# Optimization experiments

Measured on AMD Instinct MI355X. Metric: run time of the kernel, lower is better.

The kernel has to match this reference:

```python
import jax, jax.numpy as jnp
import numpy as np

PATCH_ORIG = (5, 15, 15)
DWS = [(1, 4, 4), (1, 2, 2), (1, 1, 1)]
STRIDE = [(1, 6, 6), (1, 6, 6), (1, 3, 3)]
EMBED = 32
EPS = 1e-6


def _extract_full_patches(x, shape, stride):
    # x: (N,C,D,H,W) -> (N*P, C, *shape) patches (torch unfold + permute + view)
    N, C = x.shape[:2]
    sp = x.shape[2:]
    nb = tuple((sp[i] - shape[i]) // stride[i] + 1 for i in range(3))
    d = (jnp.arange(nb[0]) * stride[0])[:, None] + jnp.arange(shape[0])[None, :]
    h = (jnp.arange(nb[1]) * stride[1])[:, None] + jnp.arange(shape[1])[None, :]
    w = (jnp.arange(nb[2]) * stride[2])[:, None] + jnp.arange(shape[2])[None, :]
    pat = x[:, :, d[:, None, None, :, None, None],
                  h[None, :, None, None, :, None],
                  w[None, None, :, None, None, :]]
    # (N, C, nb0, nb1, nb2, p0, p1, p2) -> (N*P, C, p0, p1, p2)
    pat = pat.transpose(0, 2, 3, 4, 1, 5, 6, 7).reshape(-1, C, *shape)
    return pat, nb


def _extract_centers(x, stride, offset, nb):
    # 1x1x1 patches at fixed crop offset, limited to nb -> (N*P, C)
    sl = x[:, :, offset[0]::stride[0], offset[1]::stride[1], offset[2]::stride[2]]
    sl = sl[:, :, :nb[0], :nb[1], :nb[2]]
    N, C = sl.shape[:2]
    return sl.transpose(0, 2, 3, 4, 1).reshape(-1, C)


def _maxpool(x, fct):
    # MaxPool3d(kernel=stride=fct) on exactly-divisible dims via reshape trick
    B, C = x.shape[:2]
    p0, p1, p2 = x.shape[2] // fct[0], x.shape[3] // fct[1], x.shape[4] // fct[2]
    x = x.reshape(B, C, p0, fct[0], p1, fct[1], p2, fct[2])
    return x.max(axis=(3, 5, 7))


def _dice(pred, trg):
    # inferno SorensenDiceLoss, channelwise: flatten to (C, -1)
    p = pred.transpose(1, 0, 2, 3, 4).reshape(pred.shape[1], -1)
    t = trg.transpose(1, 0, 2, 3, 4).reshape(trg.shape[1], -1)
    num = (p * t).sum(-1)
    den = jnp.clip((p * p + t * t).sum(-1), EPS, None)
    return (-2.0 * num / den).sum()


def _level_loss(pred, target, W, b, lvl):
    gt = target[:, :1].astype(jnp.float32)           # GT label volume (N,1,D,H,W)
    affs = target[:, 1:].astype(jnp.float32)
    bnd = 1.0 - affs
    bmask = bnd[:, 4:].max(1, keepdims=True) if lvl == 0 else bnd[:, :4].max(1, keepdims=True)
    dws, stride = DWS[lvl], STRIDE[lvl]
    pshape = tuple(p * f for p, f in zip(PATCH_ORIG, dws))
    off = tuple(s // 2 for s in pshape)              # crop offset (rnd crop fixed to 0)

    gt_patches, nb = _extract_full_patches(gt, pshape, stride)   # (P,1,*pshape)
    centers = _extract_centers(gt, stride, off, nb)[:, 0]        # (P,)
    on_bnd = _extract_centers(bmask, stride, off, nb)[:, 0]      # (P,)

    me = (gt_patches != centers[:, None, None, None, None]).astype(jnp.float32)
    ign = (gt_patches == 0).astype(jnp.float32)
    valid = ((centers != 0) & (on_bnd != 1.0)).astype(jnp.float32)

    trg = _maxpool(me, dws)                                      # (P,1,*PATCH_ORIG)
    ign_m = _maxpool(ign, dws) > 0

    emb = _extract_centers(pred, stride, off, nb)                # (P, EMBED)
    pp = jax.nn.sigmoid(emb @ W + b).reshape(-1, 1, *PATCH_ORIG) # patch decoder

    pp = jnp.where(ign_m, 0.0, pp)
    trg = jnp.where(ign_m, 0.0, trg)
    v = valid[:, None, None, None, None]                         # mask == select valid patches for sum-based Dice
    return _dice(pp * v, trg * v)


def setup_inputs() -> dict:
    key = jax.random.key(0)
    ks = jax.random.split(key, 16)
    shapes = [(2, 8, 160, 160), (2, 8, 80, 80), (2, 8, 40, 40)]
    inp = {}
    for lvl, (n, d, hh, ww) in enumerate(shapes):
        inp[f'pred{lvl}'] = jax.random.normal(ks[lvl], (n, EMBED, d, hh, ww), jnp.float32)
        gt = jax.random.randint(ks[3 + lvl], (n, 1, d, hh, ww), 0, 50, jnp.int32)
        affs = jax.random.randint(ks[6 + lvl], (n, 8, d, hh, ww), 0, 2, jnp.int32)
        inp[f'tgt{lvl}'] = jnp.concatenate([gt, affs], axis=1)
        inp[f'W{lvl}'] = 0.1 * jax.random.normal(ks[9 + lvl], (EMBED, int(np.prod(PATCH_ORIG))), jnp.float32)
        inp[f'b{lvl}'] = jnp.zeros((int(np.prod(PATCH_ORIG)),), jnp.float32)
    return inp


def reference(pred0, pred1, pred2, W0, b0, W1, b1, W2, b2, tgt0, tgt1, tgt2):
    loss = _level_loss(pred0, tgt0, W0, b0, 0)
    loss = loss + _level_loss(pred1, tgt1, W1, b1, 1)
    loss = loss + _level_loss(pred2, tgt2, W2, b2, 2)
    return loss
```

## Files before the change

kernel.cpp:

```cpp
#include <hip/hip_runtime.h>
#include <hip/hip_bf16.h>


constexpr int NBATCH = 2;
constexpr int EMB = 32;
constexpr int TGTC = 9;
constexpr int PZ = 5, PY = 15, PX = 15;
constexpr int P = PZ * PY * PX;

constexpr int NBLK0 = NBATCH * 4 * 17 * 17;
constexpr int NBLK1 = NBATCH * 4 * 9 * 9;
constexpr int NBLK2 = NBATCH * 4 * 9 * 9;
constexpr int NBLK_TOT = NBLK0 + NBLK1 + NBLK2;

template <int D, int H, int W,
          int NB0, int NBH, int NBW,
          int SH, int SW,
          int DH, int DWIN,
          int OFFZ, int OFFY, int OFFX,
          int AFFB>
__device__ __forceinline__
void level_body(const int lbid,
                const float* __restrict__ pred,
                const int* __restrict__ tgt,
                const float* __restrict__ Wm,
                const float* __restrict__ bv,
                float* __restrict__ partials)
{
    const int tid = threadIdx.x;

    int k  = lbid % NBW;
    int t1 = lbid / NBW;
    int j  = t1 % NBH;
    int t2 = t1 / NBH;
    int i  = t2 % NB0;
    int b  = t2 / NB0;

    const int HW = H * W;
    const int CH = D * HW;
    const int zc = OFFZ + i;
    const int yc = OFFY + j * SH;
    const int xc = OFFX + k * SW;
    const int cidx = zc * HW + yc * W + xc;

    const int c = tgt[b * TGTC * CH + cidx];
    bool allaff = true;
    #pragma unroll
    for (int ch = 0; ch < 4; ++ch)
        allaff &= (tgt[(b * TGTC + AFFB + ch) * CH + cidx] != 0);
    const bool valid = (c != 0) && allaff;

    if (!valid) {
        if (tid == 0) {
            partials[2 * lbid]     = 0.0f;
            partials[2 * lbid + 1] = 0.0f;
        }
        return;
    }

    float ev[EMB];
    #pragma unroll
    for (int e = 0; e < EMB; ++e)
        ev[e] = pred[(b * EMB + e) * CH + cidx];

    const int* __restrict__ gtb = tgt + b * TGTC * CH;

    float num = 0.0f, den = 0.0f;
    for (int o = tid; o < P; o += 256) {
        const int pz = o / (PY * PX);
        const int r  = o - pz * (PY * PX);
        const int py = r / PX;
        const int px = r - py * PX;

        float dot = bv[o];
        #pragma unroll
        for (int e = 0; e < EMB; ++e)
            dot = fmaf(ev[e], Wm[e * P + o], dot);
        float pp = __builtin_amdgcn_rcpf(1.0f + __expf(-dot));

        const int zb = i + pz;
        const int yb = j * SH + py * DH;
        const int xb = k * SW + px * DWIN;
        bool anyz = false, anyd = false;
        #pragma unroll
        for (int wy = 0; wy < DH; ++wy) {
            #pragma unroll
            for (int wx = 0; wx < DWIN; ++wx) {
                const int g = gtb[zb * HW + (yb + wy) * W + (xb + wx)];
                anyz |= (g == 0);
                anyd |= (g != c);
            }
        }
        float trg = (anyz || !anyd) ? 0.0f : 1.0f;
        if (anyz) pp = 0.0f;

        num = fmaf(pp, trg, num);
        den += pp * pp + trg * trg;
    }

    #pragma unroll
    for (int off = 32; off > 0; off >>= 1) {
        num += __shfl_xor(num, off);
        den += __shfl_xor(den, off);
    }
    __shared__ float sn[4], sd[4];
    if ((tid & 63) == 0) { sn[tid >> 6] = num; sd[tid >> 6] = den; }
    __syncthreads();
    if (tid == 0) {
        partials[2 * lbid]     = sn[0] + sn[1] + sn[2] + sn[3];
        partials[2 * lbid + 1] = sd[0] + sd[1] + sd[2] + sd[3];
    }
}

__global__ __launch_bounds__(256)
void stage_kernel(const float* __restrict__ pred0, const int* __restrict__ tgt0,
                  const float* __restrict__ W0, const float* __restrict__ b0,
                  const float* __restrict__ pred1, const int* __restrict__ tgt1,
                  const float* __restrict__ W1, const float* __restrict__ b1,
                  const float* __restrict__ pred2, const int* __restrict__ tgt2,
                  const float* __restrict__ W2, const float* __restrict__ b2,
                  float* __restrict__ partials)
{
    const int gb = blockIdx.x;
    if (gb < NBLK0) {
        level_body<8, 160, 160, 4, 17, 17, 6, 6, 4, 4, 2, 30, 30, 5>(
            gb, pred0, tgt0, W0, b0, partials);
    } else if (gb < NBLK0 + NBLK1) {
        level_body<8, 80, 80, 4, 9, 9, 6, 6, 2, 2, 2, 15, 15, 1>(
            gb - NBLK0, pred1, tgt1, W1, b1, partials + 2 * NBLK0);
    } else {
        level_body<8, 40, 40, 4, 9, 9, 3, 3, 1, 1, 2, 7, 7, 1>(
            gb - NBLK0 - NBLK1, pred2, tgt2, W2, b2,
            partials + 2 * (NBLK0 + NBLK1));
    }
}

__global__ __launch_bounds__(512)
void finalize_kernel(const float* __restrict__ partials, float* __restrict__ out)
{
    const int tid = threadIdx.x;

    constexpr int NF4 = NBLK_TOT / 2;
    constexpr int B01 = NBLK0 / 2;
    constexpr int B12 = (NBLK0 + NBLK1) / 2;

    float n0 = 0.f, d0 = 0.f, n1 = 0.f, d1 = 0.f, n2 = 0.f, d2 = 0.f;
    const float4* p4 = (const float4*)partials;
    for (int p = tid; p < NF4; p += 512) {
        const float4 v = p4[p];
        if (p < B01)      { n0 += v.x + v.z; d0 += v.y + v.w; }
        else if (p < B12) { n1 += v.x + v.z; d1 += v.y + v.w; }
        else              { n2 += v.x + v.z; d2 += v.y + v.w; }
    }

    #pragma unroll
    for (int off = 32; off > 0; off >>= 1) {
        n0 += __shfl_down(n0, off);  d0 += __shfl_down(d0, off);
        n1 += __shfl_down(n1, off);  d1 += __shfl_down(d1, off);
        n2 += __shfl_down(n2, off);  d2 += __shfl_down(d2, off);
    }
    __shared__ float s[8][6];
    if ((tid & 63) == 0) {
        const int w = tid >> 6;
        s[w][0] = n0; s[w][1] = d0; s[w][2] = n1;
        s[w][3] = d1; s[w][4] = n2; s[w][5] = d2;
    }
    __syncthreads();
    if (tid == 0) {
        float acc[6];
        #pragma unroll
        for (int q = 0; q < 6; ++q) {
            acc[q] = s[0][q];
            #pragma unroll
            for (int w = 1; w < 8; ++w) acc[q] += s[w][q];
        }
        float loss = 0.0f;
        loss += -2.0f * acc[0] / fmaxf(acc[1], 1e-6f);
        loss += -2.0f * acc[2] / fmaxf(acc[3], 1e-6f);
        loss += -2.0f * acc[4] / fmaxf(acc[5], 1e-6f);
        out[0] = loss;
    }
}

extern "C" void kernel_launch(void* const* d_in, const int* in_sizes, int n_in,
                              void* d_out, int out_size, void* d_ws, size_t ws_size,
                              hipStream_t stream)
{
    const float* pred0 = (const float*)d_in[0];
    const int*   tgt0  = (const int*)  d_in[1];
    const float* W0    = (const float*)d_in[2];
    const float* b0    = (const float*)d_in[3];
    const float* pred1 = (const float*)d_in[4];
    const int*   tgt1  = (const int*)  d_in[5];
    const float* W1    = (const float*)d_in[6];
    const float* b1    = (const float*)d_in[7];
    const float* pred2 = (const float*)d_in[8];
    const int*   tgt2  = (const int*)  d_in[9];
    const float* W2    = (const float*)d_in[10];
    const float* b2    = (const float*)d_in[11];

    float* out      = (float*)d_out;
    float* partials = (float*)d_ws;

    stage_kernel<<<NBLK_TOT, 256, 0, stream>>>(
        pred0, tgt0, W0, b0, pred1, tgt1, W1, b1, pred2, tgt2, W2, b2,
        partials);
    finalize_kernel<<<1, 512, 0, stream>>>(partials, out);
}
```

Baseline: 18.89 us.

## Merge stage and finalize into one cooperative kernel with persistent blocks

Replaces the two-kernel launch with a single cooperative kernel of 256 persistent blocks. Each block strides over several patches, checks all their validity flags up front, and runs the heavy projection only for valid ones. Per-block per-level sums are then reduced after a grid-wide sync in block 0. This removes the second launch and the work of many short-lived invalid blocks, but serialises up to SMAX patches per block, which can cause load imbalance, and adds the cost of a grid barrier.

```diff
diff --git a/kernel.cpp b/kernel.cpp
--- a/kernel.cpp
+++ b/kernel.cpp
@@ -1,5 +1,8 @@
 #include <hip/hip_runtime.h>
 #include <hip/hip_bf16.h>
+#include <hip/hip_cooperative_groups.h>
+
+namespace cg = cooperative_groups;
 
 
 constexpr int NBATCH = 2;
@@ -13,57 +16,27 @@
 constexpr int NBLK2 = NBATCH * 4 * 9 * 9;
 constexpr int NBLK_TOT = NBLK0 + NBLK1 + NBLK2;
 
-template <int D, int H, int W,
-          int NB0, int NBH, int NBW,
-          int SH, int SW,
-          int DH, int DWIN,
-          int OFFZ, int OFFY, int OFFX,
-          int AFFB>
+constexpr int GRID = 256;
+constexpr int SMAX = (NBLK_TOT + GRID - 1) / GRID;
+
+template <int Wd, int HWd, int CHd,
+          int SH, int SW, int DH, int DW,
+          int OFFY, int OFFX>
 __device__ __forceinline__
-void level_body(const int lbid,
-                const float* __restrict__ pred,
-                const int* __restrict__ tgt,
-                const float* __restrict__ Wm,
-                const float* __restrict__ bv,
-                float* __restrict__ partials)
+void heavy(const int b, const int i, const int j, const int k, const int c,
+           const float* __restrict__ pred, const int* __restrict__ tgt,
+           const float* __restrict__ Wm, const float* __restrict__ bv,
+           float& num_o, float& den_o)
 {
     const int tid = threadIdx.x;
-
-    int k  = lbid % NBW;
-    int t1 = lbid / NBW;
-    int j  = t1 % NBH;
-    int t2 = t1 / NBH;
-    int i  = t2 % NB0;
-    int b  = t2 / NB0;
-
-    const int HW = H * W;
-    const int CH = D * HW;
-    const int zc = OFFZ + i;
-    const int yc = OFFY + j * SH;
-    const int xc = OFFX + k * SW;
-    const int cidx = zc * HW + yc * W + xc;
-
-    const int c = tgt[b * TGTC * CH + cidx];
-    bool allaff = true;
-    #pragma unroll
-    for (int ch = 0; ch < 4; ++ch)
-        allaff &= (tgt[(b * TGTC + AFFB + ch) * CH + cidx] != 0);
-    const bool valid = (c != 0) && allaff;
-
-    if (!valid) {
-        if (tid == 0) {
-            partials[2 * lbid]     = 0.0f;
-            partials[2 * lbid + 1] = 0.0f;
-        }
-        return;
-    }
+    const int cidx = (2 + i) * HWd + (OFFY + j * SH) * Wd + (OFFX + k * SW);
 
     float ev[EMB];
     #pragma unroll
     for (int e = 0; e < EMB; ++e)
-        ev[e] = pred[(b * EMB + e) * CH + cidx];
-
-    const int* __restrict__ gtb = tgt + b * TGTC * CH;
+        ev[e] = pred[(b * EMB + e) * CHd + cidx];
+
+    const int* __restrict__ gtb = tgt + b * TGTC * CHd;
 
     float num = 0.0f, den = 0.0f;
     for (int o = tid; o < P; o += 256) {
@@ -80,13 +53,13 @@
 
         const int zb = i + pz;
         const int yb = j * SH + py * DH;
-        const int xb = k * SW + px * DWIN;
+        const int xb = k * SW + px * DW;
         bool anyz = false, anyd = false;
         #pragma unroll
         for (int wy = 0; wy < DH; ++wy) {
             #pragma unroll
-            for (int wx = 0; wx < DWIN; ++wx) {
-                const int g = gtb[zb * HW + (yb + wy) * W + (xb + wx)];
+            for (int wx = 0; wx < DW; ++wx) {
+                const int g = gtb[zb * HWd + (yb + wy) * Wd + (xb + wx)];
                 anyz |= (g == 0);
                 anyd |= (g != c);
             }
@@ -97,88 +70,152 @@
         num = fmaf(pp, trg, num);
         den += pp * pp + trg * trg;
     }
-
-    #pragma unroll
-    for (int off = 32; off > 0; off >>= 1) {
-        num += __shfl_xor(num, off);
-        den += __shfl_xor(den, off);
-    }
+    num_o = num;
+    den_o = den;
+}
+
+__global__ __launch_bounds__(256)
+void coop_kernel(const float* __restrict__ pred0, const int* __restrict__ tgt0,
+                 const float* __restrict__ W0, const float* __restrict__ b0,
+                 const float* __restrict__ pred1, const int* __restrict__ tgt1,
+                 const float* __restrict__ W1, const float* __restrict__ b1,
+                 const float* __restrict__ pred2, const int* __restrict__ tgt2,
+                 const float* __restrict__ W2, const float* __restrict__ b2,
+                 float* __restrict__ partials,
+                 float* __restrict__ out)
+{
+    const int bid = blockIdx.x;
+    const int tid = threadIdx.x;
+
+    __shared__ int   s_val[SMAX][5];
+    __shared__ int   s_meta[SMAX][6];
+    __shared__ int   s_flag[SMAX];
+    __shared__ int   s_list[SMAX];
+    __shared__ int   s_nv;
+    __shared__ float s_acc[6];
     __shared__ float sn[4], sd[4];
-    if ((tid & 63) == 0) { sn[tid >> 6] = num; sd[tid >> 6] = den; }
+    __shared__ float s_fin[4][6];
+
+    if (tid < 6) s_acc[tid] = 0.0f;
+
+    if (tid < SMAX * 5) {
+        const int s = tid / 5, q = tid % 5;
+        const int pb = bid + GRID * s;
+        if (pb < NBLK_TOT) {
+            int lvl, lb, NBW, NBH, Wd, HWd, CHd, offy, offx, st, affb;
+            const int* tg;
+            if (pb < NBLK0) {
+                lvl = 0; lb = pb; NBW = 17; NBH = 17;
+                Wd = 160; HWd = 25600; CHd = 204800;
+                offy = 30; offx = 30; st = 6; affb = 5; tg = tgt0;
+            } else if (pb < NBLK0 + NBLK1) {
+                lvl = 1; lb = pb - NBLK0; NBW = 9; NBH = 9;
+                Wd = 80; HWd = 6400; CHd = 51200;
+                offy = 15; offx = 15; st = 6; affb = 1; tg = tgt1;
+            } else {
+                lvl = 2; lb = pb - NBLK0 - NBLK1; NBW = 9; NBH = 9;
+                Wd = 40; HWd = 1600; CHd = 12800;
+                offy = 7; offx = 7; st = 3; affb = 1; tg = tgt2;
+            }
+            const int k  = lb % NBW;
+            const int t1 = lb / NBW;
+            const int j  = t1 % NBH;
+            const int t2 = t1 / NBH;
+            const int i  = t2 & 3;
+            const int b  = t2 >> 2;
+            const int cidx = (2 + i) * HWd + (offy + j * st) * Wd + (offx + k * st);
+            const int ch = (q == 0) ? 0 : (affb + q - 1);
+            s_val[s][q] = tg[(b * TGTC + ch) * CHd + cidx];
+            if (q == 0) {
+                s_meta[s][0] = lvl; s_meta[s][1] = b; s_meta[s][2] = i;
+                s_meta[s][3] = j;   s_meta[s][4] = k;
+            }
+        }
+    }
+    __syncthreads();
+    if (tid < SMAX) {
+        const int pb = bid + GRID * tid;
+        bool v = false;
+        if (pb < NBLK_TOT) {
+            const int c = s_val[tid][0];
+            v = (c != 0) && s_val[tid][1] && s_val[tid][2]
+                         && s_val[tid][3] && s_val[tid][4];
+            s_meta[tid][5] = c;
+        }
+        s_flag[tid] = v;
+    }
     __syncthreads();
     if (tid == 0) {
-        partials[2 * lbid]     = sn[0] + sn[1] + sn[2] + sn[3];
-        partials[2 * lbid + 1] = sd[0] + sd[1] + sd[2] + sd[3];
-    }
-}
-
-__global__ __launch_bounds__(256)
-void stage_kernel(const float* __restrict__ pred0, const int* __restrict__ tgt0,
-                  const float* __restrict__ W0, const float* __restrict__ b0,
-                  const float* __restrict__ pred1, const int* __restrict__ tgt1,
-                  const float* __restrict__ W1, const float* __restrict__ b1,
-                  const float* __restrict__ pred2, const int* __restrict__ tgt2,
-                  const float* __restrict__ W2, const float* __restrict__ b2,
-                  float* __restrict__ partials)
-{
-    const int gb = blockIdx.x;
-    if (gb < NBLK0) {
-        level_body<8, 160, 160, 4, 17, 17, 6, 6, 4, 4, 2, 30, 30, 5>(
-            gb, pred0, tgt0, W0, b0, partials);
-    } else if (gb < NBLK0 + NBLK1) {
-        level_body<8, 80, 80, 4, 9, 9, 6, 6, 2, 2, 2, 15, 15, 1>(
-            gb - NBLK0, pred1, tgt1, W1, b1, partials + 2 * NBLK0);
-    } else {
-        level_body<8, 40, 40, 4, 9, 9, 3, 3, 1, 1, 2, 7, 7, 1>(
-            gb - NBLK0 - NBLK1, pred2, tgt2, W2, b2,
-            partials + 2 * (NBLK0 + NBLK1));
-    }
-}
-
-__global__ __launch_bounds__(512)
-void finalize_kernel(const float* __restrict__ partials, float* __restrict__ out)
-{
-    const int tid = threadIdx.x;
-
-    constexpr int NF4 = NBLK_TOT / 2;
-    constexpr int B01 = NBLK0 / 2;
-    constexpr int B12 = (NBLK0 + NBLK1) / 2;
-
-    float n0 = 0.f, d0 = 0.f, n1 = 0.f, d1 = 0.f, n2 = 0.f, d2 = 0.f;
-    const float4* p4 = (const float4*)partials;
-    for (int p = tid; p < NF4; p += 512) {
-        const float4 v = p4[p];
-        if (p < B01)      { n0 += v.x + v.z; d0 += v.y + v.w; }
-        else if (p < B12) { n1 += v.x + v.z; d1 += v.y + v.w; }
-        else              { n2 += v.x + v.z; d2 += v.y + v.w; }
-    }
-
-    #pragma unroll
-    for (int off = 32; off > 0; off >>= 1) {
-        n0 += __shfl_down(n0, off);  d0 += __shfl_down(d0, off);
-        n1 += __shfl_down(n1, off);  d1 += __shfl_down(d1, off);
-        n2 += __shfl_down(n2, off);  d2 += __shfl_down(d2, off);
-    }
-    __shared__ float s[8][6];
-    if ((tid & 63) == 0) {
-        const int w = tid >> 6;
-        s[w][0] = n0; s[w][1] = d0; s[w][2] = n1;
-        s[w][3] = d1; s[w][4] = n2; s[w][5] = d2;
+        int n = 0;
+        #pragma unroll
+        for (int s = 0; s < SMAX; ++s)
+            if (s_flag[s]) s_list[n++] = s;
+        s_nv = n;
     }
     __syncthreads();
-    if (tid == 0) {
-        float acc[6];
-        #pragma unroll
-        for (int q = 0; q < 6; ++q) {
-            acc[q] = s[0][q];
+
+    const int nv = s_nv;
+    for (int v = 0; v < nv; ++v) {
+        const int s   = s_list[v];
+        const int lvl = s_meta[s][0], b = s_meta[s][1], i = s_meta[s][2];
+        const int j   = s_meta[s][3], k = s_meta[s][4], c = s_meta[s][5];
+
+        float num, den;
+        if (lvl == 0)
+            heavy<160, 25600, 204800, 6, 6, 4, 4, 30, 30>(
+                b, i, j, k, c, pred0, tgt0, W0, b0, num, den);
+        else if (lvl == 1)
+            heavy<80, 6400, 51200, 6, 6, 2, 2, 15, 15>(
+                b, i, j, k, c, pred1, tgt1, W1, b1, num, den);
+        else
+            heavy<40, 1600, 12800, 3, 3, 1, 1, 7, 7>(
+                b, i, j, k, c, pred2, tgt2, W2, b2, num, den);
+
+        #pragma unroll
+        for (int off = 32; off > 0; off >>= 1) {
+            num += __shfl_xor(num, off);
+            den += __shfl_xor(den, off);
+        }
+        if ((tid & 63) == 0) { sn[tid >> 6] = num; sd[tid >> 6] = den; }
+        __syncthreads();
+        if (tid == 0) {
+            s_acc[2 * lvl]     += sn[0] + sn[1] + sn[2] + sn[3];
+            s_acc[2 * lvl + 1] += sd[0] + sd[1] + sd[2] + sd[3];
+        }
+        __syncthreads();
+    }
+
+    if (tid < 6) partials[bid * 6 + tid] = s_acc[tid];
+
+    cg::this_grid().sync();
+
+    if (bid == 0) {
+        const float* p = partials + tid * 6;
+        float n0 = p[0], d0 = p[1], n1 = p[2], d1 = p[3], n2 = p[4], d2 = p[5];
+
+        #pragma unroll
+        for (int off = 32; off > 0; off >>= 1) {
+            n0 += __shfl_xor(n0, off);  d0 += __shfl_xor(d0, off);
+            n1 += __shfl_xor(n1, off);  d1 += __shfl_xor(d1, off);
+            n2 += __shfl_xor(n2, off);  d2 += __shfl_xor(d2, off);
+        }
+        if ((tid & 63) == 0) {
+            const int w = tid >> 6;
+            s_fin[w][0] = n0; s_fin[w][1] = d0; s_fin[w][2] = n1;
+            s_fin[w][3] = d1; s_fin[w][4] = n2; s_fin[w][5] = d2;
+        }
+        __syncthreads();
+        if (tid == 0) {
+            float a[6];
             #pragma unroll
-            for (int w = 1; w < 8; ++w) acc[q] += s[w][q];
-        }
-        float loss = 0.0f;
-        loss += -2.0f * acc[0] / fmaxf(acc[1], 1e-6f);
-        loss += -2.0f * acc[2] / fmaxf(acc[3], 1e-6f);
-        loss += -2.0f * acc[4] / fmaxf(acc[5], 1e-6f);
-        out[0] = loss;
+            for (int q = 0; q < 6; ++q)
+                a[q] = s_fin[0][q] + s_fin[1][q] + s_fin[2][q] + s_fin[3][q];
+            float loss = 0.0f;
+            loss += -2.0f * a[0] / fmaxf(a[1], 1e-6f);
+            loss += -2.0f * a[2] / fmaxf(a[3], 1e-6f);
+            loss += -2.0f * a[4] / fmaxf(a[5], 1e-6f);
+            out[0] = loss;
+        }
     }
 }
 
@@ -202,8 +239,12 @@
     float* out      = (float*)d_out;
     float* partials = (float*)d_ws;
 
-    stage_kernel<<<NBLK_TOT, 256, 0, stream>>>(
-        pred0, tgt0, W0, b0, pred1, tgt1, W1, b1, pred2, tgt2, W2, b2,
-        partials);
-    finalize_kernel<<<1, 512, 0, stream>>>(partials, out);
+    void* args[] = {
+        (void*)&pred0, (void*)&tgt0, (void*)&W0, (void*)&b0,
+        (void*)&pred1, (void*)&tgt1, (void*)&W1, (void*)&b1,
+        (void*)&pred2, (void*)&tgt2, (void*)&W2, (void*)&b2,
+        (void*)&partials, (void*)&out
+    };
+    hipLaunchCooperativeKernel((const void*)coop_kernel,
+                               dim3(GRID), dim3(256), args, 0, stream);
 }
```

After: 67.76 us. 259% more time.

## Fuse finalize into stage kernel via sentinel-polling last block

Applied to the files above, without the earlier changes.

Merges the reduction kernel into the main kernel. An extra block spins on the partials buffer, which a memset pre-fills with a sentinel value, until every slot has been written, then reduces the slots and writes the loss. The aim is to remove the second kernel launch and its gap. In exchange it adds a memset launch and relies on the polling block making progress while the other blocks run. A block that is scheduled early and spins costs CU time, and the scheme assumes no partial ever legitimately has the sentinel bit pattern (a NaN).

```diff
diff --git a/kernel.cpp b/kernel.cpp
--- a/kernel.cpp
+++ b/kernel.cpp
@@ -12,6 +12,13 @@
 constexpr int NBLK1 = NBATCH * 4 * 9 * 9;
 constexpr int NBLK2 = NBATCH * 4 * 9 * 9;
 constexpr int NBLK_TOT = NBLK0 + NBLK1 + NBLK2;
+
+constexpr unsigned int SENT = 0xFFFFFFFFu;
+
+__device__ __forceinline__ void slot_store(float* p, float v)
+{
+    __hip_atomic_store(p, v, __ATOMIC_RELAXED, __HIP_MEMORY_SCOPE_AGENT);
+}
 
 template <int D, int H, int W,
           int NB0, int NBH, int NBW,
@@ -52,8 +59,8 @@
 
     if (!valid) {
         if (tid == 0) {
-            partials[2 * lbid]     = 0.0f;
-            partials[2 * lbid + 1] = 0.0f;
+            slot_store(&partials[2 * lbid],     0.0f);
+            slot_store(&partials[2 * lbid + 1], 0.0f);
         }
         return;
     }
@@ -107,50 +114,67 @@
     if ((tid & 63) == 0) { sn[tid >> 6] = num; sd[tid >> 6] = den; }
     __syncthreads();
     if (tid == 0) {
-        partials[2 * lbid]     = sn[0] + sn[1] + sn[2] + sn[3];
-        partials[2 * lbid + 1] = sd[0] + sd[1] + sd[2] + sd[3];
+        slot_store(&partials[2 * lbid],
+                   sn[0] + sn[1] + sn[2] + sn[3]);
+        slot_store(&partials[2 * lbid + 1],
+                   sd[0] + sd[1] + sd[2] + sd[3]);
     }
 }
 
 __global__ __launch_bounds__(256)
-void stage_kernel(const float* __restrict__ pred0, const int* __restrict__ tgt0,
+void fused_kernel(const float* __restrict__ pred0, const int* __restrict__ tgt0,
                   const float* __restrict__ W0, const float* __restrict__ b0,
                   const float* __restrict__ pred1, const int* __restrict__ tgt1,
                   const float* __restrict__ W1, const float* __restrict__ b1,
                   const float* __restrict__ pred2, const int* __restrict__ tgt2,
                   const float* __restrict__ W2, const float* __restrict__ b2,
-                  float* __restrict__ partials)
+                  float* __restrict__ partials,
+                  float* __restrict__ out)
 {
     const int gb = blockIdx.x;
+    const int tid = threadIdx.x;
+
     if (gb < NBLK0) {
         level_body<8, 160, 160, 4, 17, 17, 6, 6, 4, 4, 2, 30, 30, 5>(
             gb, pred0, tgt0, W0, b0, partials);
+        return;
     } else if (gb < NBLK0 + NBLK1) {
         level_body<8, 80, 80, 4, 9, 9, 6, 6, 2, 2, 2, 15, 15, 1>(
             gb - NBLK0, pred1, tgt1, W1, b1, partials + 2 * NBLK0);
-    } else {
+        return;
+    } else if (gb < NBLK_TOT) {
         level_body<8, 40, 40, 4, 9, 9, 3, 3, 1, 1, 2, 7, 7, 1>(
             gb - NBLK0 - NBLK1, pred2, tgt2, W2, b2,
             partials + 2 * (NBLK0 + NBLK1));
-    }
-}
-
-__global__ __launch_bounds__(512)
-void finalize_kernel(const float* __restrict__ partials, float* __restrict__ out)
-{
-    const int tid = threadIdx.x;
-
-    constexpr int NF4 = NBLK_TOT / 2;
-    constexpr int B01 = NBLK0 / 2;
-    constexpr int B12 = (NBLK0 + NBLK1) / 2;
+        return;
+    }
+
+    __shared__ int s_any;
+    const unsigned int* pw = (const unsigned int*)partials;
+    for (;;) {
+        if (tid == 0) s_any = 0;
+        __syncthreads();
+        bool any = false;
+        for (int w = tid; w < NBLK_TOT * 2; w += 256) {
+            const unsigned int v = __hip_atomic_load(
+                pw + w, __ATOMIC_RELAXED, __HIP_MEMORY_SCOPE_AGENT);
+            any |= (v == SENT);
+        }
+        if (any) s_any = 1;
+        __syncthreads();
+        if (!s_any) break;
+        __builtin_amdgcn_s_sleep(16);
+    }
 
     float n0 = 0.f, d0 = 0.f, n1 = 0.f, d1 = 0.f, n2 = 0.f, d2 = 0.f;
-    const float4* p4 = (const float4*)partials;
-    for (int p = tid; p < NF4; p += 512) {
-        const float4 v = p4[p];
-        if (p < B01)      { n0 += v.x + v.z; d0 += v.y + v.w; }
-        else if (p < B12) { n1 += v.x + v.z; d1 += v.y + v.w; }
-        else              { n2 += v.x + v.z; d2 += v.y + v.w; }
+    for (int p = tid; p < NBLK_TOT; p += 256) {
+        const float nx = __hip_atomic_load(partials + 2 * p,
+                                           __ATOMIC_RELAXED, __HIP_MEMORY_SCOPE_AGENT);
+        const float dx = __hip_atomic_load(partials + 2 * p + 1,
+                                           __ATOMIC_RELAXED, __HIP_MEMORY_SCOPE_AGENT);
+        if (p < NBLK0)              { n0 += nx; d0 += dx; }
+        else if (p < NBLK0 + NBLK1) { n1 += nx; d1 += dx; }
+        else                        { n2 += nx; d2 += dx; }
     }
 
     #pragma unroll
@@ -159,7 +183,7 @@
         n1 += __shfl_down(n1, off);  d1 += __shfl_down(d1, off);
         n2 += __shfl_down(n2, off);  d2 += __shfl_down(d2, off);
     }
-    __shared__ float s[8][6];
+    __shared__ float s[4][6];
     if ((tid & 63) == 0) {
         const int w = tid >> 6;
         s[w][0] = n0; s[w][1] = d0; s[w][2] = n1;
@@ -167,17 +191,14 @@
     }
     __syncthreads();
     if (tid == 0) {
-        float acc[6];
+        float a[6];
         #pragma unroll
-        for (int q = 0; q < 6; ++q) {
-            acc[q] = s[0][q];
-            #pragma unroll
-            for (int w = 1; w < 8; ++w) acc[q] += s[w][q];
-        }
+        for (int q = 0; q < 6; ++q)
+            a[q] = s[0][q] + s[1][q] + s[2][q] + s[3][q];
         float loss = 0.0f;
-        loss += -2.0f * acc[0] / fmaxf(acc[1], 1e-6f);
-        loss += -2.0f * acc[2] / fmaxf(acc[3], 1e-6f);
-        loss += -2.0f * acc[4] / fmaxf(acc[5], 1e-6f);
+        loss += -2.0f * a[0] / fmaxf(a[1], 1e-6f);
+        loss += -2.0f * a[2] / fmaxf(a[3], 1e-6f);
+        loss += -2.0f * a[4] / fmaxf(a[5], 1e-6f);
         out[0] = loss;
     }
 }
@@ -202,8 +223,9 @@
     float* out      = (float*)d_out;
     float* partials = (float*)d_ws;
 
-    stage_kernel<<<NBLK_TOT, 256, 0, stream>>>(
+    hipMemsetAsync(partials, 0xFF, NBLK_TOT * 2 * sizeof(float), stream);
+
+    fused_kernel<<<NBLK_TOT + 1, 256, 0, stream>>>(
         pred0, tgt0, W0, b0, pred1, tgt1, W1, b1, pred2, tgt2, W2, b2,
-        partials);
-    finalize_kernel<<<1, 512, 0, stream>>>(partials, out);
-}
+        partials, out);
+}
```

Measured after the change: 29.24 us. 1.55x slower.
